# Kernel optimization log

Measured on AMD Instinct MI355X. Metric: run time of the kernel, lower is better.

The kernel has to match this reference:

```python
import jax, jax.numpy as jnp
import numpy as np

N = 50000; E = 1600000; W = 12; CIN = 32; CMID = 32; COUT = 32; K = 2; KER = 3; DIL = 1


def setup_inputs() -> dict:
    key = jax.random.key(0)
    ks = jax.random.split(key, 6)
    x = jax.random.normal(ks[0], (W, N, CIN), jnp.float32)
    A = jax.random.randint(ks[1], (2, E), 0, N, jnp.int32)
    Ew = jax.random.uniform(ks[2], (E,), jnp.float32)
    Wcheb = jax.random.normal(ks[3], (W, K, CIN, CMID), jnp.float32) / np.sqrt(CIN)
    bcheb = jnp.zeros((W, CMID), jnp.float32)
    Wconv = jax.random.normal(ks[4], (COUT, CMID, KER), jnp.float32) / np.sqrt(CMID * KER)
    bconv = jnp.zeros((COUT,), jnp.float32)
    return dict(x=x, A=A, Ew=Ew, Wcheb=Wcheb, bcheb=bcheb, Wconv=Wconv, bconv=bconv, batch_size=1)


def _prop(x, src, dst, w_hat):
    # one sparse matvec with L_hat per timestep; x: [W, N, C]
    msg = x[:, src, :] * w_hat[None, :, None]                      # [W, E, C]
    agg = jax.ops.segment_sum(msg.transpose(1, 0, 2), dst, num_segments=x.shape[1])  # [N, W, C]
    return agg.transpose(1, 0, 2)                                  # [W, N, C]


def reference(x, A, Ew, Wcheb, bcheb, Wconv, bconv, batch_size):
    src, dst = A[0], A[1]
    # sym-normalized Laplacian with lambda_max=2: L_hat = -D^{-1/2} A D^{-1/2}
    deg = jax.ops.segment_sum(Ew, dst, num_segments=x.shape[1])
    dinv = jnp.where(deg > 0, jax.lax.rsqrt(jnp.maximum(deg, 1e-12)), 0.0)
    w_hat = -dinv[src] * Ew * dinv[dst]

    # Chebyshev recurrence (vectorized over all window_size graphs at once)
    Txs = [x, _prop(x, src, dst, w_hat)]
    for _ in range(Wcheb.shape[1] - 2):
        Txs.append(2.0 * _prop(Txs[-1], src, dst, w_hat) - Txs[-2])

    out = bcheb[:, None, :]                                        # [W, 1, CMID]
    for k, Txk in enumerate(Txs):
        out = out + jnp.einsum('wnc,wcd->wnd', Txk, Wcheb[:, k])   # per-timestep weights

    # temporal Conv1d over the window axis: nodes act as conv batch
    h = out.transpose(1, 2, 0)                                     # [N, CMID, W]
    pad = (KER // 2) * DIL
    h = jax.lax.conv_general_dilated(h, Wconv, (1,), [(pad, pad)], rhs_dilation=(DIL,),
                                     dimension_numbers=('NCH', 'OIH', 'NCH'))
    h = h + bconv[None, :, None]
    h = h.transpose(0, 2, 1)                                       # [N, W, COUT]
    h = jnp.where(h >= 0, h, 0.01 * h)                             # LeakyReLU; dropout p=0 is identity
    return h
```

## Files before the change

kernel.cpp:

```cpp
#include <hip/hip_runtime.h>

#define WW 12
#define CH 32
#define KERN 3
#define ROWB 384
#define EBLK 8192

typedef __attribute__((ext_vector_type(8))) short short8v;
typedef __attribute__((ext_vector_type(4))) short short4v;
typedef __attribute__((ext_vector_type(4))) float f32x4;

__device__ __forceinline__ unsigned short bf16rne(float v) {
  unsigned int u = __float_as_uint(v);
  return (unsigned short)((u + 0x7FFFu + ((u >> 16) & 1u)) >> 16);
}
__device__ __forceinline__ float bf16tof(unsigned int b) {
  return __uint_as_float(b << 16);
}

__device__ __forceinline__ unsigned char fp8e4m3(float x) {
  unsigned int u = __float_as_uint(x);
  unsigned int s = (u >> 24) & 0x80u;
  float ax = fabsf(x);
  if (ax >= 464.f) return (unsigned char)(s | 0x7E);
  if (ax < 0.015625f) {
    int m = __float2int_rn(ax * 512.f);
    return (unsigned char)(s | (unsigned)m);
  }
  unsigned int au = u & 0x7fffffffu;
  au += 0x7FFFFu + ((au >> 20) & 1u);
  int e = (int)(au >> 23) - 127 + 7;
  unsigned int m = (au >> 20) & 7u;
  if (e > 15 || (e == 15 && m == 7)) return (unsigned char)(s | 0x7E);
  return (unsigned char)(s | ((unsigned)e << 3) | m);
}

__device__ __forceinline__ void dec4fma(unsigned int u, float wh, float* acc) {
#if __has_builtin(__builtin_amdgcn_cvt_pk_f32_fp8)
  auto lo = __builtin_amdgcn_cvt_pk_f32_fp8((int)u, false);
  auto hi = __builtin_amdgcn_cvt_pk_f32_fp8((int)u, true);
  acc[0] = fmaf(wh, lo[0], acc[0]);
  acc[1] = fmaf(wh, lo[1], acc[1]);
  acc[2] = fmaf(wh, hi[0], acc[2]);
  acc[3] = fmaf(wh, hi[1], acc[3]);
#else
#pragma unroll
  for (int j = 0; j < 4; ++j) {
    unsigned int b = (u >> (8 * j)) & 0xffu;
    float f = __uint_as_float(((b & 0x80u) << 24) | ((b & 0x7fu) << 20)) * 0x1.0p120f;
    acc[j] = fmaf(wh, f, acc[j]);
  }
#endif
}

__global__ __launch_bounds__(256) void histA_kernel(const int* __restrict__ dst,
                                                    int* __restrict__ blockhist,
                                                    int E, int NB) {
  __shared__ unsigned int hist[256];
  const int b = blockIdx.x;
  const int tid = threadIdx.x;
  hist[tid] = 0;
  __syncthreads();
  const int base = b * EBLK;
#pragma unroll
  for (int k = 0; k < EBLK / 256; ++k) {
    int e = base + k * 256 + tid;
    if (e < E) atomicAdd(&hist[(unsigned)dst[e] >> 8], 1u);
  }
  __syncthreads();
  blockhist[tid * NB + b] = (int)hist[tid];
}

__global__ void scanA_kernel(const int* __restrict__ in, int* __restrict__ bsum, int M) {
  __shared__ int red[256];
  int i = blockIdx.x * 256 + threadIdx.x;
  red[threadIdx.x] = (i < M) ? in[i] : 0;
  __syncthreads();
  for (int o = 128; o > 0; o >>= 1) {
    if (threadIdx.x < o) red[threadIdx.x] += red[threadIdx.x + o];
    __syncthreads();
  }
  if (threadIdx.x == 0) bsum[blockIdx.x] = red[0];
}
__global__ void scanB_kernel(int* __restrict__ bsum, int nb) {
  __shared__ int tmp[256];
  int tid = threadIdx.x;
  int v = (tid < nb) ? bsum[tid] : 0;
  tmp[tid] = v;
  __syncthreads();
  for (int o = 1; o < 256; o <<= 1) {
    int t = (tid >= o) ? tmp[tid - o] : 0;
    __syncthreads();
    tmp[tid] += t;
    __syncthreads();
  }
  if (tid < nb) bsum[tid] = tmp[tid] - v;
}
__global__ void scanC_kernel(const int* __restrict__ in, const int* __restrict__ bsum,
                             int* __restrict__ out, int M) {
  __shared__ int tmp[256];
  int tid = threadIdx.x;
  int i = blockIdx.x * 256 + tid;
  int v = (i < M) ? in[i] : 0;
  tmp[tid] = v;
  __syncthreads();
  for (int o = 1; o < 256; o <<= 1) {
    int t = (tid >= o) ? tmp[tid - o] : 0;
    __syncthreads();
    tmp[tid] += t;
    __syncthreads();
  }
  if (i < M) out[i] = bsum[blockIdx.x] + tmp[tid] - v;
}

__global__ __launch_bounds__(256) void scatpack_kernel(
    const int* __restrict__ src, const int* __restrict__ dst, const float* __restrict__ Ew,
    const int* __restrict__ scanout, unsigned long long* __restrict__ rec8,
    const float* __restrict__ x, const float* __restrict__ Wcheb,
    const float* __restrict__ Wconv,
    unsigned short* __restrict__ xt, unsigned char* __restrict__ xq,
    unsigned short* __restrict__ wb01, unsigned short* __restrict__ wbc,
    int E, int N, int NB, int npackTot, int npx) {
  const int group = blockIdx.x / 49;
  const int slot = blockIdx.x % 49;
  if (slot == 48) {
    const int b = group;
    if (b >= NB) return;
    __shared__ unsigned int hist[256];
    const int tid = threadIdx.x;
    hist[tid] = 0;
    __syncthreads();
    const int base = b * EBLK;
#pragma unroll
    for (int k = 0; k < EBLK / 256; ++k) {
      int e = base + k * 256 + tid;
      if (e < E) {
        int d = dst[e];
        int bucket = (unsigned)d >> 8;
        unsigned int lr = atomicAdd(&hist[bucket], 1u);
        int pos = scanout[bucket * NB + b] + (int)lr;
        unsigned long long rec = ((unsigned long long)(unsigned)d << 32) |
                                 ((unsigned)src[e] << 16) | bf16rne(Ew[e]);
        rec8[pos] = rec;
      }
    }
    return;
  }
  int pid = group * 48 + slot;
  if (pid >= npackTot) return;
  if (pid < npx) {
    long long f = ((long long)pid * 256 + threadIdx.x) * 8;
    const long long T = (long long)WW * N * CH;
    if (f >= T) return;
    float4 v0 = *(const float4*)(x + f);
    float4 v1 = *(const float4*)(x + f + 4);
    int w = (int)(f / ((long long)N * CH));
    int rem = (int)(f - (long long)w * N * CH);
    int n = rem >> 5;
    int c = rem & 31;
    size_t o = (size_t)n * ROWB + w * CH + c;
    short4v h0, h1;
    h0[0] = (short)bf16rne(v0.x); h0[1] = (short)bf16rne(v0.y);
    h0[2] = (short)bf16rne(v0.z); h0[3] = (short)bf16rne(v0.w);
    h1[0] = (short)bf16rne(v1.x); h1[1] = (short)bf16rne(v1.y);
    h1[2] = (short)bf16rne(v1.z); h1[3] = (short)bf16rne(v1.w);
    *(short4v*)(xt + o) = h0;
    *(short4v*)(xt + o + 4) = h1;
    unsigned int q0 = (unsigned int)fp8e4m3(v0.x) | ((unsigned int)fp8e4m3(v0.y) << 8) |
                      ((unsigned int)fp8e4m3(v0.z) << 16) | ((unsigned int)fp8e4m3(v0.w) << 24);
    unsigned int q1 = (unsigned int)fp8e4m3(v1.x) | ((unsigned int)fp8e4m3(v1.y) << 8) |
                      ((unsigned int)fp8e4m3(v1.z) << 16) | ((unsigned int)fp8e4m3(v1.w) << 24);
    *(unsigned int*)(xq + o) = q0;
    *(unsigned int*)(xq + o + 4) = q1;
    return;
  }
  int id = (pid - npx) * 256 + threadIdx.x;
  if (id < 12 * 2 * 2 * 64 * 8) {
    int j = id & 7, l = (id >> 3) & 63, h = (id >> 9) & 1, m = (id >> 10) & 1, ww = id >> 11;
    int k = ((l >> 4) << 3) + j;
    int d = (l & 15) + (h << 4);
    wb01[id] = bf16rne(Wcheb[((size_t)(ww * 2 + m) * 32 + k) * 32 + d]);
  } else if (id < 24576 + 3 * 2 * 64 * 8) {
    int i2 = id - 24576;
    int j = i2 & 7, l = (i2 >> 3) & 63, h = (i2 >> 9) & 1, k = i2 >> 10;
    int c = ((l >> 4) << 3) + j;
    int o = (l & 15) + (h << 4);
    wbc[i2] = bf16rne(Wconv[((size_t)(o * 32 + c)) * 3 + k]);
  }
}

__global__ __launch_bounds__(256) void passB_kernel(
    const unsigned long long* __restrict__ rec8, const int* __restrict__ scanout,
    int* __restrict__ rowptr, float* __restrict__ dinv,
    unsigned int* __restrict__ epair, int N, int E, int NB) {
  __shared__ unsigned int hist[256];
  __shared__ unsigned int qsum[256];
  __shared__ int sub[256];
  __shared__ int tmp[256];
  const int B = blockIdx.x;
  const int tid = threadIdx.x;
  hist[tid] = 0;
  qsum[tid] = 0;
  __syncthreads();
  const int bstart = scanout[B * NB];
  const int bend = scanout[(B + 1) * NB];
  for (int i = bstart + tid; i < bend; i += 256) {
    unsigned long long r = rec8[i];
    int low = (int)((r >> 32) & 255u);
    atomicAdd(&hist[low], 1u);
    unsigned int q = (unsigned int)__float2int_rn(bf16tof((unsigned int)r & 0xffffu) * 16777216.f);
    atomicAdd(&qsum[low], q);
  }
  __syncthreads();
  int v = (int)hist[tid];
  tmp[tid] = v;
  __syncthreads();
  for (int o = 1; o < 256; o <<= 1) {
    int t = (tid >= o) ? tmp[tid - o] : 0;
    __syncthreads();
    tmp[tid] += t;
    __syncthreads();
  }
  sub[tid] = tmp[tid] - v;
  int n = (B << 8) + tid;
  if (n < N) {
    rowptr[n] = bstart + sub[tid];
    float deg = (float)qsum[tid] * (1.f / 16777216.f);
    dinv[n] = (deg > 0.f) ? rsqrtf(fmaxf(deg, 1e-12f)) : 0.f;
  }
  if (B == 0 && tid == 0) rowptr[N] = E;
  hist[tid] = 0;
  __syncthreads();
  for (int i = bstart + tid; i < bend; i += 256) {
    unsigned long long r = rec8[i];
    int low = (int)((r >> 32) & 255u);
    unsigned int lr = atomicAdd(&hist[low], 1u);
    epair[bstart + sub[low] + (int)lr] = (unsigned int)r;
  }
}

__global__ __launch_bounds__(256) void gather_kernel(
    const int* __restrict__ rowptr, const unsigned int* __restrict__ epair,
    const float* __restrict__ dinv,
    const unsigned char* __restrict__ xq, unsigned short* __restrict__ zt, int N) {
  int gt = blockIdx.x * blockDim.x + threadIdx.x;
  int n = gt >> 6;
  if (n >= N) return;
  int lane = gt & 63;
  int half = lane >> 5;
  int l = lane & 31;

  const float ndinv = -dinv[n];

  float acc[WW];
#pragma unroll
  for (int j = 0; j < WW; ++j) acc[j] = 0.f;

  int i = rowptr[n] + half;
  const int i1 = rowptr[n + 1];
  for (; i + 6 < i1; i += 8) {
    unsigned int e0 = epair[i];
    unsigned int e1 = epair[i + 2];
    unsigned int e2 = epair[i + 4];
    unsigned int e3 = epair[i + 6];
    const unsigned int* p0 = (const unsigned int*)(xq + (size_t)(e0 >> 16) * ROWB + l * 12);
    const unsigned int* p1 = (const unsigned int*)(xq + (size_t)(e1 >> 16) * ROWB + l * 12);
    const unsigned int* p2 = (const unsigned int*)(xq + (size_t)(e2 >> 16) * ROWB + l * 12);
    const unsigned int* p3 = (const unsigned int*)(xq + (size_t)(e3 >> 16) * ROWB + l * 12);
    unsigned int a0 = p0[0], a1 = p0[1], a2 = p0[2];
    unsigned int b0 = p1[0], b1 = p1[1], b2 = p1[2];
    unsigned int c0 = p2[0], c1 = p2[1], c2 = p2[2];
    unsigned int d0 = p3[0], d1 = p3[1], d2 = p3[2];
    float w0 = ndinv * bf16tof(e0 & 0xffffu) * dinv[e0 >> 16];
    float w1 = ndinv * bf16tof(e1 & 0xffffu) * dinv[e1 >> 16];
    float w2 = ndinv * bf16tof(e2 & 0xffffu) * dinv[e2 >> 16];
    float w3 = ndinv * bf16tof(e3 & 0xffffu) * dinv[e3 >> 16];
    dec4fma(a0, w0, acc + 0); dec4fma(a1, w0, acc + 4); dec4fma(a2, w0, acc + 8);
    dec4fma(b0, w1, acc + 0); dec4fma(b1, w1, acc + 4); dec4fma(b2, w1, acc + 8);
    dec4fma(c0, w2, acc + 0); dec4fma(c1, w2, acc + 4); dec4fma(c2, w2, acc + 8);
    dec4fma(d0, w3, acc + 0); dec4fma(d1, w3, acc + 4); dec4fma(d2, w3, acc + 8);
  }
  for (; i < i1; i += 2) {
    unsigned int e0 = epair[i];
    const unsigned int* p0 = (const unsigned int*)(xq + (size_t)(e0 >> 16) * ROWB + l * 12);
    unsigned int a0 = p0[0], a1 = p0[1], a2 = p0[2];
    float w0 = ndinv * bf16tof(e0 & 0xffffu) * dinv[e0 >> 16];
    dec4fma(a0, w0, acc + 0); dec4fma(a1, w0, acc + 4); dec4fma(a2, w0, acc + 8);
  }
#pragma unroll
  for (int j = 0; j < WW; ++j) acc[j] += __shfl_xor(acc[j], 32);

  if (half == 0) {
    unsigned short* q = zt + (size_t)n * ROWB + l * 12;
    short4v o0, o1, o2;
#pragma unroll
    for (int j = 0; j < 4; ++j) {
      o0[j] = (short)bf16rne(acc[j]);
      o1[j] = (short)bf16rne(acc[4 + j]);
      o2[j] = (short)bf16rne(acc[8 + j]);
    }
    *(short4v*)(q) = o0;
    *(short4v*)(q + 4) = o1;
    *(short4v*)(q + 8) = o2;
  }
}

__global__ __launch_bounds__(256) void mc_kernel(
    const unsigned short* __restrict__ xt, const unsigned short* __restrict__ zt,
    const unsigned short* __restrict__ wb01, const unsigned short* __restrict__ wbc,
    const float* __restrict__ bcheb, const float* __restrict__ bconv,
    float* __restrict__ out, int N) {
  __shared__ __align__(16) unsigned short hts[4][4][16][40];
  const int wid = threadIdx.x >> 6;
  const int lane = threadIdx.x & 63;
  const int n0 = (blockIdx.x * 4 + wid) * 16;
  if (n0 >= N) return;
  const int kg = lane >> 4;
  const int arow = lane & 15;
  const int rrow = min(n0 + arow, N - 1);

  short8v wcf0[3], wcf1[3];
#pragma unroll
  for (int k = 0; k < 3; ++k) {
    wcf0[k] = *(const short8v*)(wbc + (((k * 2 + 0) * 64 + lane) << 3));
    wcf1[k] = *(const short8v*)(wbc + (((k * 2 + 1) * 64 + lane) << 3));
  }
  const float bc0 = bconv[arow];
  const float bc1 = bconv[arow + 16];

  auto computeH = [&](int w) {
    const size_t fofs = (size_t)rrow * ROWB + w * CH + kg * 8;
    short8v xf = *(const short8v*)(xt + fofs);
    short8v zf = *(const short8v*)(zt + fofs);
    unsigned short* hrow = &hts[wid][w & 3][0][0];
#pragma unroll
    for (int h = 0; h < 2; ++h) {
      short8v w0f = *(const short8v*)(wb01 + ((((w * 2 + 0) * 2 + h) * 64 + lane) << 3));
      short8v w1f = *(const short8v*)(wb01 + ((((w * 2 + 1) * 2 + h) * 64 + lane) << 3));
      f32x4 acc = {0.f, 0.f, 0.f, 0.f};
      acc = __builtin_amdgcn_mfma_f32_16x16x32_bf16(xf, w0f, acc, 0, 0, 0);
      acc = __builtin_amdgcn_mfma_f32_16x16x32_bf16(zf, w1f, acc, 0, 0, 0);
      const int d = arow + (h << 4);
      const float bias = bcheb[w * CH + d];
#pragma unroll
      for (int r = 0; r < 4; ++r) {
        hrow[(kg * 4 + r) * 40 + d] = bf16rne(acc[r] + bias);
      }
    }
  };

  auto convT = [&](int t) {
    f32x4 a0 = {0.f, 0.f, 0.f, 0.f};
    f32x4 a1 = {0.f, 0.f, 0.f, 0.f};
#pragma unroll
    for (int k = 0; k < 3; ++k) {
      int w = t + k - 1;
      if (w < 0 || w >= WW) continue;
      short8v hf = *(const short8v*)(&hts[wid][w & 3][arow][kg * 8]);
      a0 = __builtin_amdgcn_mfma_f32_16x16x32_bf16(hf, wcf0[k], a0, 0, 0, 0);
      a1 = __builtin_amdgcn_mfma_f32_16x16x32_bf16(hf, wcf1[k], a1, 0, 0, 0);
    }
#pragma unroll
    for (int r = 0; r < 4; ++r) {
      int node = n0 + kg * 4 + r;
      if (node >= N) continue;
      float v0 = a0[r] + bc0;
      float v1 = a1[r] + bc1;
      v0 = (v0 >= 0.f) ? v0 : 0.01f * v0;
      v1 = (v1 >= 0.f) ? v1 : 0.01f * v1;
      size_t o = ((size_t)node * WW + t) * CH;
      out[o + arow] = v0;
      out[o + arow + 16] = v1;
    }
  };

  computeH(0);
  computeH(1);
  convT(0);
  for (int w = 2; w < WW; ++w) {
    computeH(w);
    convT(w - 1);
  }
  convT(WW - 1);
}

extern "C" void kernel_launch(void* const* d_in, const int* in_sizes, int n_in,
                              void* d_out, int out_size, void* d_ws, size_t ws_size,
                              hipStream_t stream) {
  const float* x     = (const float*)d_in[0];
  const int*   A     = (const int*)d_in[1];
  const float* Ew    = (const float*)d_in[2];
  const float* Wcheb = (const float*)d_in[3];
  const float* bcheb = (const float*)d_in[4];
  const float* Wconv = (const float*)d_in[5];
  const float* bconv = (const float*)d_in[6];
  float* out = (float*)d_out;

  const int E = in_sizes[2];
  const int N = in_sizes[0] / (WW * CH);
  const int* srcA = A;
  const int* dstA = A + E;

  char* ws = (char*)d_ws;
  size_t off = 0;
  auto alloc = [&](size_t bytes) -> void* {
    void* p = ws + off;
    off += (bytes + 255) / 256 * 256;
    return p;
  };
  const int NB = (E + EBLK - 1) / EBLK;
  const int M = 256 * NB;
  const int NBUCK = (N + 255) / 256;

  int* blockhist = (int*)alloc((size_t)M * 4);
  int* scanout   = (int*)alloc((size_t)(M + 1) * 4);
  int* bsum      = (int*)alloc((size_t)256 * 4);
  int* rowptr    = (int*)alloc((size_t)(N + 1) * 4);
  float* dinv    = (float*)alloc((size_t)N * 4);
  unsigned long long* rec8 = (unsigned long long*)alloc((size_t)E * 8);
  unsigned int* epair = (unsigned int*)alloc((size_t)E * 4);
  unsigned short* xt   = (unsigned short*)alloc((size_t)N * ROWB * 2);
  unsigned char*  xq   = (unsigned char*)alloc((size_t)N * ROWB);
  unsigned short* zt   = (unsigned short*)alloc((size_t)N * ROWB * 2);
  unsigned short* wb01 = (unsigned short*)alloc((size_t)24576 * 2);
  unsigned short* wbc  = (unsigned short*)alloc((size_t)3072 * 2);
  (void)ws_size;

  histA_kernel<<<NB, 256, 0, stream>>>(dstA, blockhist, E, NB);

  const int nbs = (M + 255) / 256;
  scanA_kernel<<<nbs, 256, 0, stream>>>(blockhist, bsum, M);
  scanB_kernel<<<1, 256, 0, stream>>>(bsum, nbs);
  scanC_kernel<<<nbs, 256, 0, stream>>>(blockhist, bsum, scanout, M);

  const long long T = (long long)WW * N * CH;
  const int npx = (int)((T + 2047) / 2048);
  const int nwb = (24576 + 3072 + 255) / 256;
  const int npackTot = npx + nwb;
  const int ngroups = max(NB, (npackTot + 47) / 48);
  scatpack_kernel<<<ngroups * 49, 256, 0, stream>>>(
      srcA, dstA, Ew, scanout, rec8, x, Wcheb, Wconv, xt, xq, wb01, wbc,
      E, N, NB, npackTot, npx);

  passB_kernel<<<NBUCK, 256, 0, stream>>>(rec8, scanout, rowptr, dinv, epair, N, E, NB);

  long long gtot = (long long)N * 64;
  gather_kernel<<<(unsigned)((gtot + 255) / 256), 256, 0, stream>>>(rowptr, epair, dinv, xq, zt, N);

  int ntiles = (N + 15) / 16;
  int mcblocks = (ntiles + 3) / 4;
  mc_kernel<<<mcblocks, 256, 0, stream>>>(xt, zt, wb01, wbc, bcheb, bconv, out, N);
}
```

Before: 253.0 us.

## Shrink edge blocks, generalize block-sum scan, software-prefetch edge records

Cuts edges per scatter block from 8192 to 2048, so the histogram and scatter phase runs on four times as many blocks. It rewrites scanB so one block can scan more than 256 partial sums, and sizes bsum to match. Scatter blocks now come first in a flat grid instead of being interleaved one per 49 blocks. The scatter and passB loops also prefetch the next edge record to hide load latency. The trade-off is a larger histogram and scan (four times as many entries) and more scanout reads per bucket.

Result: faster. 220.3 us (-12.9%).

```diff
diff --git a/kernel.cpp b/kernel.cpp
--- a/kernel.cpp
+++ b/kernel.cpp
@@ -4,7 +4,7 @@
 #define CH 32
 #define KERN 3
 #define ROWB 384
-#define EBLK 8192
+#define EBLK 2048
 
 typedef __attribute__((ext_vector_type(8))) short short8v;
 typedef __attribute__((ext_vector_type(4))) short short4v;
@@ -85,8 +85,11 @@
 __global__ void scanB_kernel(int* __restrict__ bsum, int nb) {
   __shared__ int tmp[256];
   int tid = threadIdx.x;
-  int v = (tid < nb) ? bsum[tid] : 0;
-  tmp[tid] = v;
+  int chunk = (nb + 255) / 256;
+  int lo = tid * chunk, hi = min(lo + chunk, nb);
+  int s = 0;
+  for (int i = lo; i < hi; ++i) s += bsum[i];
+  tmp[tid] = s;
   __syncthreads();
   for (int o = 1; o < 256; o <<= 1) {
     int t = (tid >= o) ? tmp[tid - o] : 0;
@@ -94,7 +97,12 @@
     tmp[tid] += t;
     __syncthreads();
   }
-  if (tid < nb) bsum[tid] = tmp[tid] - v;
+  int run = tmp[tid] - s;
+  for (int i = lo; i < hi; ++i) {
+    int v = bsum[i];
+    bsum[i] = run;
+    run += v;
+  }
 }
 __global__ void scanC_kernel(const int* __restrict__ in, const int* __restrict__ bsum,
                              int* __restrict__ out, int M) {
@@ -121,32 +129,36 @@
     unsigned short* __restrict__ xt, unsigned char* __restrict__ xq,
     unsigned short* __restrict__ wb01, unsigned short* __restrict__ wbc,
     int E, int N, int NB, int npackTot, int npx) {
-  const int group = blockIdx.x / 49;
-  const int slot = blockIdx.x % 49;
-  if (slot == 48) {
-    const int b = group;
-    if (b >= NB) return;
+  if ((int)blockIdx.x < NB) {
+    const int b = blockIdx.x;
     __shared__ unsigned int hist[256];
     const int tid = threadIdx.x;
     hist[tid] = 0;
     __syncthreads();
-    const int base = b * EBLK;
+    int e = b * EBLK + tid;
+    bool valid = e < E;
+    int d = 0, s = 0;
+    float w = 0.f;
+    if (valid) { d = dst[e]; s = src[e]; w = Ew[e]; }
 #pragma unroll
     for (int k = 0; k < EBLK / 256; ++k) {
-      int e = base + k * 256 + tid;
-      if (e < E) {
-        int d = dst[e];
+      int e2 = e + 256;
+      bool v2 = (k + 1 < EBLK / 256) && (e2 < E);
+      int d2 = 0, s2 = 0;
+      float w2 = 0.f;
+      if (v2) { d2 = dst[e2]; s2 = src[e2]; w2 = Ew[e2]; }
+      if (valid) {
         int bucket = (unsigned)d >> 8;
         unsigned int lr = atomicAdd(&hist[bucket], 1u);
         int pos = scanout[bucket * NB + b] + (int)lr;
-        unsigned long long rec = ((unsigned long long)(unsigned)d << 32) |
-                                 ((unsigned)src[e] << 16) | bf16rne(Ew[e]);
-        rec8[pos] = rec;
+        rec8[pos] = ((unsigned long long)(unsigned)d << 32) |
+                    ((unsigned)s << 16) | bf16rne(w);
       }
+      e = e2; d = d2; s = s2; w = w2; valid = v2;
     }
     return;
   }
-  int pid = group * 48 + slot;
+  int pid = blockIdx.x - NB;
   if (pid >= npackTot) return;
   if (pid < npx) {
     long long f = ((long long)pid * 256 + threadIdx.x) * 8;
@@ -204,12 +216,18 @@
   __syncthreads();
   const int bstart = scanout[B * NB];
   const int bend = scanout[(B + 1) * NB];
-  for (int i = bstart + tid; i < bend; i += 256) {
-    unsigned long long r = rec8[i];
-    int low = (int)((r >> 32) & 255u);
-    atomicAdd(&hist[low], 1u);
-    unsigned int q = (unsigned int)__float2int_rn(bf16tof((unsigned int)r & 0xffffu) * 16777216.f);
-    atomicAdd(&qsum[low], q);
+  {
+    int i = bstart + tid;
+    unsigned long long r = (i < bend) ? rec8[i] : 0;
+    while (i < bend) {
+      int i2 = i + 256;
+      unsigned long long r2 = (i2 < bend) ? rec8[i2] : 0;
+      int low = (int)((r >> 32) & 255u);
+      atomicAdd(&hist[low], 1u);
+      unsigned int q = (unsigned int)__float2int_rn(bf16tof((unsigned int)r & 0xffffu) * 16777216.f);
+      atomicAdd(&qsum[low], q);
+      i = i2; r = r2;
+    }
   }
   __syncthreads();
   int v = (int)hist[tid];
@@ -231,11 +249,17 @@
   if (B == 0 && tid == 0) rowptr[N] = E;
   hist[tid] = 0;
   __syncthreads();
-  for (int i = bstart + tid; i < bend; i += 256) {
-    unsigned long long r = rec8[i];
-    int low = (int)((r >> 32) & 255u);
-    unsigned int lr = atomicAdd(&hist[low], 1u);
-    epair[bstart + sub[low] + (int)lr] = (unsigned int)r;
+  {
+    int i = bstart + tid;
+    unsigned long long r = (i < bend) ? rec8[i] : 0;
+    while (i < bend) {
+      int i2 = i + 256;
+      unsigned long long r2 = (i2 < bend) ? rec8[i2] : 0;
+      int low = (int)((r >> 32) & 255u);
+      unsigned int lr = atomicAdd(&hist[low], 1u);
+      epair[bstart + sub[low] + (int)lr] = (unsigned int)r;
+      i = i2; r = r2;
+    }
   }
 }
 
@@ -414,7 +438,7 @@
 
   int* blockhist = (int*)alloc((size_t)M * 4);
   int* scanout   = (int*)alloc((size_t)(M + 1) * 4);
-  int* bsum      = (int*)alloc((size_t)256 * 4);
+  int* bsum      = (int*)alloc((size_t)((M + 255) / 256) * 4);
   int* rowptr    = (int*)alloc((size_t)(N + 1) * 4);
   float* dinv    = (float*)alloc((size_t)N * 4);
   unsigned long long* rec8 = (unsigned long long*)alloc((size_t)E * 8);
@@ -437,8 +461,7 @@
   const int npx = (int)((T + 2047) / 2048);
   const int nwb = (24576 + 3072 + 255) / 256;
   const int npackTot = npx + nwb;
-  const int ngroups = max(NB, (npackTot + 47) / 48);
-  scatpack_kernel<<<ngroups * 49, 256, 0, stream>>>(
+  scatpack_kernel<<<NB + npackTot, 256, 0, stream>>>(
       srcA, dstA, Ew, scanout, rec8, x, Wcheb, Wconv, xt, xq, wb01, wbc,
       E, N, NB, npackTot, npx);
 
```
